# Optimization experiments

Measured on AMD Instinct MI355X. Metric: run time of the kernel, lower is better.

Reference implementation:

```python
import jax, jax.numpy as jnp
import numpy as np

EMBED_DIM = 128
NUM_CLASSES = 2
NUM_NODES = 100000
NUM_EDGES = 500000


def setup_inputs() -> dict:
    key = jax.random.key(0)
    k1, k2, k3, k4, k5, k6 = jax.random.split(key, 6)
    node_embed = jax.random.normal(k1, (NUM_NODES, EMBED_DIM), dtype=jnp.float32)
    edge_index = jax.random.randint(k2, (2, NUM_EDGES), 0, NUM_NODES, dtype=jnp.int64)
    # MLP params (torch Linear default init scale ~ 1/sqrt(fan_in))
    s1 = 1.0 / np.sqrt(2 * EMBED_DIM)
    s2 = 1.0 / np.sqrt(EMBED_DIM)
    W1 = jax.random.uniform(k3, (2 * EMBED_DIM, EMBED_DIM), jnp.float32, -s1, s1)
    b1 = jax.random.uniform(k4, (EMBED_DIM,), jnp.float32, -s1, s1)
    W2 = jax.random.uniform(k5, (EMBED_DIM, NUM_CLASSES), jnp.float32, -s2, s2)
    b2 = jax.random.uniform(k6, (NUM_CLASSES,), jnp.float32, -s2, s2)
    return {"node_embed": node_embed, "edge_index": edge_index,
            "W1": W1, "b1": b1, "W2": W2, "b2": b2}


def reference(node_embed, edge_index, W1, b1, W2, b2):
    row, col = edge_index[0], edge_index[1]
    # Gather endpoint embeddings and concat -> [num_edges, 2*embed_dim]
    edge_feat = jnp.concatenate([node_embed[row], node_embed[col]], axis=1)
    h = jax.nn.relu(edge_feat @ W1 + b1)  # [num_edges, embed_dim]
    # Dropout(0.1) is identity in eval mode.
    return h @ W2 + b2  # [num_edges, num_classes]
```

## Files before the change

### kernel.cpp

```cpp
#include <hip/hip_runtime.h>
#include <hip/hip_bf16.h>


#define EMBED 128

typedef _Float16 half8 __attribute__((ext_vector_type(8)));
typedef _Float16 half4 __attribute__((ext_vector_type(4)));
typedef float floatx4 __attribute__((ext_vector_type(4)));

__global__ __launch_bounds__(256) void prep(
    const float* __restrict__ W1, const float* __restrict__ W2,
    const float* __restrict__ b1, const int* __restrict__ idx,
    _Float16* __restrict__ WT, _Float16* __restrict__ W2PT,
    _Float16* __restrict__ b1f, int* __restrict__ flag) {
    if (blockIdx.x < 128) {
        __shared__ float lds[16][17];
        const int ty = threadIdx.x >> 4, tx = threadIdx.x & 15;
        const int r0 = (blockIdx.x >> 3) * 16;
        const int c0 = (blockIdx.x & 7) * 16;
        lds[ty][tx] = W1[(r0 + ty) * 128 + c0 + tx];
        __syncthreads();
        const int jbase = c0 + (r0 >= 128 ? 128 : 0);
        const int kbase = r0 & 127;
        WT[(size_t)(jbase + ty) * 128 + kbase + tx] = (_Float16)lds[tx][ty];
    } else {
        const int t = threadIdx.x;
        if (t < 64) {
            const int hw = idx[2 * t + 1];
            const unsigned long long m = __ballot(hw != 0);
            if (t == 0) *flag = (m == 0ull) ? 1 : 0;
        }
        if (t < 128) b1f[t] = (_Float16)b1[t];
        for (int i = t; i < 2048; i += 256) {
            const int n = i >> 7, k = i & 127;
            W2PT[i] = (n < 2) ? (_Float16)W2[k * 2 + n] : (_Float16)0.f;
        }
    }
}

__global__ __launch_bounds__(256) void gemm_ab(
    const float* __restrict__ X, const _Float16* __restrict__ WT,
    _Float16* __restrict__ AB, int n_nodes) {
    __shared__ _Float16 xs[64 * 136];
    const int t = threadIdx.x;
    const int mblk = blockIdx.x * 64;

#pragma unroll
    for (int i = 0; i < 8; ++i) {
        const int flat = i * 1024 + t * 4;
        const int row = flat >> 7, col = flat & 127;
        int node = mblk + row;
        if (node > n_nodes - 1) node = n_nodes - 1;
        const float4 v = *(const float4*)(X + (size_t)node * EMBED + col);
        half4 h;
        h[0] = (_Float16)v.x; h[1] = (_Float16)v.y;
        h[2] = (_Float16)v.z; h[3] = (_Float16)v.w;
        *(half4*)(xs + row * 136 + col) = h;
    }
    __syncthreads();

    const int w = t >> 6, lane = t & 63, lm = lane & 15, quad = lane >> 4;

    floatx4 acc[4][4];
#pragma unroll
    for (int a = 0; a < 4; ++a)
#pragma unroll
        for (int b = 0; b < 4; ++b)
            acc[a][b] = (floatx4){0.f, 0.f, 0.f, 0.f};

#pragma unroll
    for (int ks = 0; ks < 4; ++ks) {
        const int k0 = ks * 32 + quad * 8;
        half8 xf[4];
#pragma unroll
        for (int mf = 0; mf < 4; ++mf)
            xf[mf] = *(const half8*)(xs + (mf * 16 + lm) * 136 + k0);
#pragma unroll
        for (int jf = 0; jf < 4; ++jf) {
            const int j = w * 64 + jf * 16 + lm;
            const half8 wf = *(const half8*)(WT + (size_t)j * EMBED + k0);
#pragma unroll
            for (int mf = 0; mf < 4; ++mf)
                acc[mf][jf] = __builtin_amdgcn_mfma_f32_16x16x32_f16(wf, xf[mf], acc[mf][jf], 0, 0, 0);
        }
    }

#pragma unroll
    for (int mf = 0; mf < 4; ++mf) {
        const int node = mblk + mf * 16 + lm;
        if (node < n_nodes) {
#pragma unroll
            for (int jf = 0; jf < 4; ++jf) {
                half4 h;
#pragma unroll
                for (int r = 0; r < 4; ++r) h[r] = (_Float16)acc[mf][jf][r];
                *(half4*)(AB + (size_t)node * 256 + w * 64 + jf * 16 + quad * 4) = h;
            }
        }
    }
}

__global__ __launch_bounds__(256) void edge_mlp(
    const _Float16* __restrict__ AB, const int* __restrict__ eidx,
    const int* __restrict__ flag, const _Float16* __restrict__ b1f,
    const _Float16* __restrict__ W2PT, const float* __restrict__ b2,
    float* __restrict__ out, int n_edges) {
    const int lane = threadIdx.x & 63, lm = lane & 15, quad = lane >> 4;
    const int ebase = (blockIdx.x * 4 + (threadIdx.x >> 6)) * 32;
    if (ebase >= n_edges) return;

    const int mode = *flag;
    int e0 = ebase + lm, e1 = ebase + 16 + lm;
    if (e0 > n_edges - 1) e0 = n_edges - 1;
    if (e1 > n_edges - 1) e1 = n_edges - 1;
    int row0, col0, row1, col1;
    if (mode) {
        row0 = eidx[2 * (size_t)e0];
        col0 = eidx[2 * ((size_t)n_edges + e0)];
        row1 = eidx[2 * (size_t)e1];
        col1 = eidx[2 * ((size_t)n_edges + e1)];
    } else {
        row0 = eidx[e0];
        col0 = eidx[(size_t)n_edges + e0];
        row1 = eidx[e1];
        col1 = eidx[(size_t)n_edges + e1];
    }

    const _Float16* a0p = AB + (size_t)row0 * 256;
    const _Float16* b0p = AB + (size_t)col0 * 256 + 128;
    const _Float16* a1p = AB + (size_t)row1 * 256;
    const _Float16* b1p = AB + (size_t)col1 * 256 + 128;

    half8 a0[4], b0[4], a1[4], b1[4];
#pragma unroll
    for (int ks = 0; ks < 4; ++ks) {
        const int k0 = ks * 32 + quad * 8;
        a0[ks] = *(const half8*)(a0p + k0);
        b0[ks] = *(const half8*)(b0p + k0);
        a1[ks] = *(const half8*)(a1p + k0);
        b1[ks] = *(const half8*)(b1p + k0);
    }

    floatx4 acc0 = (floatx4){0.f, 0.f, 0.f, 0.f};
    floatx4 acc1 = (floatx4){0.f, 0.f, 0.f, 0.f};
#pragma unroll
    for (int ks = 0; ks < 4; ++ks) {
        const int k0 = ks * 32 + quad * 8;
        const half8 bi = *(const half8*)(b1f + k0);
        const half8 wv = *(const half8*)(W2PT + lm * 128 + k0);
        half8 h0 = a0[ks] + b0[ks] + bi;
        half8 h1 = a1[ks] + b1[ks] + bi;
#pragma unroll
        for (int j = 0; j < 8; ++j) {
            h0[j] = h0[j] > (_Float16)0.f ? h0[j] : (_Float16)0.f;
            h1[j] = h1[j] > (_Float16)0.f ? h1[j] : (_Float16)0.f;
        }
        acc0 = __builtin_amdgcn_mfma_f32_16x16x32_f16(h0, wv, acc0, 0, 0, 0);
        acc1 = __builtin_amdgcn_mfma_f32_16x16x32_f16(h1, wv, acc1, 0, 0, 0);
    }

    if (lm < 2) {
        const float b2v = b2[lm];
#pragma unroll
        for (int r = 0; r < 4; ++r) {
            const int ed0 = ebase + quad * 4 + r;
            const int ed1 = ebase + 16 + quad * 4 + r;
            if (ed0 < n_edges) out[(size_t)ed0 * 2 + lm] = acc0[r] + b2v;
            if (ed1 < n_edges) out[(size_t)ed1 * 2 + lm] = acc1[r] + b2v;
        }
    }
}

extern "C" void kernel_launch(void* const* d_in, const int* in_sizes, int n_in,
                              void* d_out, int out_size, void* d_ws, size_t ws_size,
                              hipStream_t stream) {
    const float* X   = (const float*)d_in[0];
    const int*   idx = (const int*)d_in[1];
    const float* W1  = (const float*)d_in[2];
    const float* b1  = (const float*)d_in[3];
    const float* W2  = (const float*)d_in[4];
    const float* b2  = (const float*)d_in[5];
    float* out = (float*)d_out;

    const int n_nodes = in_sizes[0] / EMBED;
    const int n_edges = in_sizes[1] / 2;

    char* ws = (char*)d_ws;
    int*      flag = (int*)ws;
    _Float16* AB   = (_Float16*)(ws + 256);
    _Float16* WT   = (_Float16*)(ws + 256 + (size_t)n_nodes * 512);
    _Float16* W2PT = WT + 256 * 128;
    _Float16* b1f  = W2PT + 16 * 128;

    prep<<<129, 256, 0, stream>>>(W1, W2, b1, idx, WT, W2PT, b1f, flag);
    gemm_ab<<<(n_nodes + 63) / 64, 256, 0, stream>>>(X, WT, AB, n_nodes);
    edge_mlp<<<(n_edges + 127) / 128, 256, 0, stream>>>(
        AB, idx, flag, b1f, W2PT, b2, out, n_edges);
}
```

Before: 165.9 us.

## Load node rows straight into MFMA fragments and stage output through LDS

```diff
diff --git a/kernel.cpp b/kernel.cpp
--- a/kernel.cpp
+++ b/kernel.cpp
@@ -41,62 +41,67 @@
 __global__ __launch_bounds__(256) void gemm_ab(
     const float* __restrict__ X, const _Float16* __restrict__ WT,
     _Float16* __restrict__ AB, int n_nodes) {
-    __shared__ _Float16 xs[64 * 136];
+    __shared__ _Float16 outs[4][32 * 136];
     const int t = threadIdx.x;
-    const int mblk = blockIdx.x * 64;
-
-#pragma unroll
-    for (int i = 0; i < 8; ++i) {
-        const int flat = i * 1024 + t * 4;
-        const int row = flat >> 7, col = flat & 127;
-        int node = mblk + row;
-        if (node > n_nodes - 1) node = n_nodes - 1;
-        const float4 v = *(const float4*)(X + (size_t)node * EMBED + col);
-        half4 h;
-        h[0] = (_Float16)v.x; h[1] = (_Float16)v.y;
-        h[2] = (_Float16)v.z; h[3] = (_Float16)v.w;
-        *(half4*)(xs + row * 136 + col) = h;
-    }
-    __syncthreads();
-
-    const int w = t >> 6, lane = t & 63, lm = lane & 15, quad = lane >> 4;
-
-    floatx4 acc[4][4];
-#pragma unroll
-    for (int a = 0; a < 4; ++a)
-#pragma unroll
-        for (int b = 0; b < 4; ++b)
+    const int wv = t >> 6, lane = t & 63, lm = lane & 15, quad = lane >> 4;
+    const int base    = blockIdx.x * 64 + (wv >> 1) * 32;
+    const int colbase = (wv & 1) * 128;
+
+    int r0 = base + lm;      if (r0 > n_nodes - 1) r0 = n_nodes - 1;
+    int r1 = base + 16 + lm; if (r1 > n_nodes - 1) r1 = n_nodes - 1;
+    const float* x0 = X + (size_t)r0 * EMBED;
+    const float* x1 = X + (size_t)r1 * EMBED;
+    const _Float16* wtp = WT + (size_t)(colbase + lm) * EMBED;
+
+    floatx4 acc[2][8];
+#pragma unroll
+    for (int a = 0; a < 2; ++a)
+#pragma unroll
+        for (int b = 0; b < 8; ++b)
             acc[a][b] = (floatx4){0.f, 0.f, 0.f, 0.f};
 
 #pragma unroll
     for (int ks = 0; ks < 4; ++ks) {
         const int k0 = ks * 32 + quad * 8;
-        half8 xf[4];
-#pragma unroll
-        for (int mf = 0; mf < 4; ++mf)
-            xf[mf] = *(const half8*)(xs + (mf * 16 + lm) * 136 + k0);
-#pragma unroll
-        for (int jf = 0; jf < 4; ++jf) {
-            const int j = w * 64 + jf * 16 + lm;
-            const half8 wf = *(const half8*)(WT + (size_t)j * EMBED + k0);
-#pragma unroll
-            for (int mf = 0; mf < 4; ++mf)
-                acc[mf][jf] = __builtin_amdgcn_mfma_f32_16x16x32_f16(wf, xf[mf], acc[mf][jf], 0, 0, 0);
-        }
-    }
-
-#pragma unroll
-    for (int mf = 0; mf < 4; ++mf) {
-        const int node = mblk + mf * 16 + lm;
-        if (node < n_nodes) {
-#pragma unroll
-            for (int jf = 0; jf < 4; ++jf) {
-                half4 h;
-#pragma unroll
-                for (int r = 0; r < 4; ++r) h[r] = (_Float16)acc[mf][jf][r];
-                *(half4*)(AB + (size_t)node * 256 + w * 64 + jf * 16 + quad * 4) = h;
-            }
-        }
+        const float4 a0 = *(const float4*)(x0 + k0);
+        const float4 a1 = *(const float4*)(x0 + k0 + 4);
+        const float4 c0 = *(const float4*)(x1 + k0);
+        const float4 c1 = *(const float4*)(x1 + k0 + 4);
+        half8 xf0, xf1;
+        xf0[0] = (_Float16)a0.x; xf0[1] = (_Float16)a0.y;
+        xf0[2] = (_Float16)a0.z; xf0[3] = (_Float16)a0.w;
+        xf0[4] = (_Float16)a1.x; xf0[5] = (_Float16)a1.y;
+        xf0[6] = (_Float16)a1.z; xf0[7] = (_Float16)a1.w;
+        xf1[0] = (_Float16)c0.x; xf1[1] = (_Float16)c0.y;
+        xf1[2] = (_Float16)c0.z; xf1[3] = (_Float16)c0.w;
+        xf1[4] = (_Float16)c1.x; xf1[5] = (_Float16)c1.y;
+        xf1[6] = (_Float16)c1.z; xf1[7] = (_Float16)c1.w;
+#pragma unroll
+        for (int jf = 0; jf < 8; ++jf) {
+            const half8 wf = *(const half8*)(wtp + (size_t)jf * 16 * EMBED + k0);
+            acc[0][jf] = __builtin_amdgcn_mfma_f32_16x16x32_f16(wf, xf0, acc[0][jf], 0, 0, 0);
+            acc[1][jf] = __builtin_amdgcn_mfma_f32_16x16x32_f16(wf, xf1, acc[1][jf], 0, 0, 0);
+        }
+    }
+
+    _Float16* o = outs[wv];
+#pragma unroll
+    for (int mf = 0; mf < 2; ++mf) {
+#pragma unroll
+        for (int jf = 0; jf < 8; ++jf) {
+            half4 h;
+#pragma unroll
+            for (int r = 0; r < 4; ++r) h[r] = (_Float16)acc[mf][jf][r];
+            *(half4*)(o + (mf * 16 + lm) * 136 + jf * 16 + quad * 4) = h;
+        }
+    }
+#pragma unroll
+    for (int i = 0; i < 8; ++i) {
+        const int nl = i * 4 + (lane >> 4);
+        const int gnode = base + nl;
+        const half8 v = *(const half8*)(o + nl * 136 + lm * 8);
+        if (gnode < n_nodes)
+            *(half8*)(AB + (size_t)gnode * 256 + colbase + lm * 8) = v;
     }
 }
 
```

Measured after the change: 176.8 us. 6.5% more time.
